# Performance work log

Hardware: AMD Instinct MI355X
Metric: run time of the kernel (lower is better)

Reference implementation:

```python
import jax, jax.numpy as jnp
import numpy as np

N = 100000
E = 3200000
F_IN = 128


def gcn_conv(x, w, b, src, dst, n):
    """PyG GCNConv: out = D^-1/2 (A + I) D^-1/2 (x @ w) + b.
    src/dst already include self loops."""
    xw = x @ w                                   # [N, F_out]
    ones = jnp.ones(src.shape[0], dtype=xw.dtype)
    deg = jax.ops.segment_sum(ones, dst, num_segments=n)   # in-degree incl. self loop
    dinv = jnp.where(deg > 0, jax.lax.rsqrt(deg), 0.0)
    norm = dinv[src] * dinv[dst]                 # [E+N]
    msg = xw[src] * norm[:, None]                # gather + scale
    out = jax.ops.segment_sum(msg, dst, num_segments=n)
    return out + b


def setup_inputs() -> dict:
    key = jax.random.key(0)
    ks = jax.random.split(key, 10)
    x = jax.random.normal(ks[0], (N, F_IN), dtype=jnp.float32)
    edge_index = jax.random.randint(ks[1], (2, E), 0, N, dtype=jnp.int64)
    # Glorot-ish init for weights
    def lin(k, fi, fo):
        return jax.random.normal(k, (fi, fo), dtype=jnp.float32) / np.sqrt(fi)
    return {
        "x": x,
        "edge_index": edge_index,
        "w1": lin(ks[2], F_IN, 64), "b1": jnp.zeros((64,), jnp.float32),
        "w2": lin(ks[3], 64, 32),   "b2": jnp.zeros((32,), jnp.float32),
        "w3": lin(ks[4], 32, 16),   "b3": jnp.zeros((16,), jnp.float32),
        "w_out": lin(ks[5], 16, 1), "b_out": jnp.zeros((1,), jnp.float32),
    }


def reference(x, edge_index, w1, b1, w2, b2, w3, b3, w_out, b_out):
    n = x.shape[0]
    # add self loops once (PyG adds them inside each GCNConv; same graph => same result)
    loop = jnp.arange(n, dtype=edge_index.dtype)
    src = jnp.concatenate([edge_index[0], loop])
    dst = jnp.concatenate([edge_index[1], loop])
    h = jax.nn.relu(gcn_conv(x, w1, b1, src, dst, n))
    h = jax.nn.relu(gcn_conv(h, w2, b2, src, dst, n))
    h = jax.nn.relu(gcn_conv(h, w3, b3, src, dst, n))
    return h @ w_out + b_out  # [N, 1]
```

## Files before the change

### kernel.cpp

```cpp
#include <hip/hip_runtime.h>
#include <hip/hip_bf16.h>


#define NBUCK 391
#define BSHIFT 8
#define CAP 10240
#define TILE 4096

typedef __attribute__((ext_vector_type(2))) unsigned short ushort2v;
typedef __attribute__((ext_vector_type(4))) unsigned short ushort4v;
typedef __attribute__((ext_vector_type(8))) unsigned short ushort8v;
typedef __attribute__((ext_vector_type(8))) _Float16 half8;
typedef __attribute__((ext_vector_type(4))) float f32x4;

__device__ __forceinline__ float bf2f(unsigned short u) {
  union { unsigned int i; float f; } v;
  v.i = ((unsigned int)u) << 16;
  return v.f;
}
__device__ __forceinline__ unsigned short f2bf(float f) {
  union { float f; unsigned int i; } v;
  v.f = f;
  unsigned int r = v.i + 0x7FFF + ((v.i >> 16) & 1);
  return (unsigned short)(r >> 16);
}

static __global__ __launch_bounds__(256) void partition_kernel(
    const int* __restrict__ src, const int* __restrict__ dst,
    int* __restrict__ bucket_cnt, int* __restrict__ part, int E) {
  __shared__ int sorted[TILE];
  __shared__ int hist[512];
  __shared__ int lstart[512];
  __shared__ int cur[512];
  __shared__ int gbase[512];
  __shared__ int sdata[256];
  const int t = threadIdx.x;
  const int base0 = blockIdx.x * TILE;
  hist[t] = 0;
  hist[t + 256] = 0;
  __syncthreads();
  for (int i = t * 4; i < TILE; i += 1024) {
    int gi = base0 + i;
    if (gi + 4 <= E) {
      int4 d = *(const int4*)&dst[gi];
      atomicAdd(&hist[d.x >> BSHIFT], 1);
      atomicAdd(&hist[d.y >> BSHIFT], 1);
      atomicAdd(&hist[d.z >> BSHIFT], 1);
      atomicAdd(&hist[d.w >> BSHIFT], 1);
    } else {
      for (int k = 0; k < 4 && gi + k < E; ++k)
        atomicAdd(&hist[dst[gi + k] >> BSHIFT], 1);
    }
  }
  __syncthreads();
  const int v0 = hist[2 * t], v1 = hist[2 * t + 1];
  const int s = v0 + v1;
  sdata[t] = s;
  __syncthreads();
  int incl = s;
  for (int off = 1; off < 256; off <<= 1) {
    int y = (t >= off) ? sdata[t - off] : 0;
    __syncthreads();
    incl += y;
    sdata[t] = incl;
    __syncthreads();
  }
  const int excl = incl - s;
  lstart[2 * t] = excl;
  lstart[2 * t + 1] = excl + v0;
  cur[2 * t] = 0;
  cur[2 * t + 1] = 0;
  if (2 * t < NBUCK && v0) gbase[2 * t] = atomicAdd(&bucket_cnt[2 * t], v0);
  if (2 * t + 1 < NBUCK && v1)
    gbase[2 * t + 1] = atomicAdd(&bucket_cnt[2 * t + 1], v1);
  __syncthreads();
  for (int i = t * 4; i < TILE; i += 1024) {
    int gi = base0 + i;
    if (gi + 4 <= E) {
      int4 d = *(const int4*)&dst[gi];
      int4 sc = *(const int4*)&src[gi];
      int b0 = d.x >> BSHIFT, b1 = d.y >> BSHIFT;
      int b2 = d.z >> BSHIFT, b3 = d.w >> BSHIFT;
      int p0 = lstart[b0] + atomicAdd(&cur[b0], 1);
      sorted[p0] = ((d.x & 255) << 17) | sc.x;
      int p1 = lstart[b1] + atomicAdd(&cur[b1], 1);
      sorted[p1] = ((d.y & 255) << 17) | sc.y;
      int p2 = lstart[b2] + atomicAdd(&cur[b2], 1);
      sorted[p2] = ((d.z & 255) << 17) | sc.z;
      int p3 = lstart[b3] + atomicAdd(&cur[b3], 1);
      sorted[p3] = ((d.w & 255) << 17) | sc.w;
    } else {
      for (int k = 0; k < 4 && gi + k < E; ++k) {
        int d = dst[gi + k], sc = src[gi + k];
        int b = d >> BSHIFT;
        int pos = lstart[b] + atomicAdd(&cur[b], 1);
        sorted[pos] = ((d & 255) << 17) | sc;
      }
    }
  }
  __syncthreads();
  for (int b = t; b < NBUCK; b += 256) {
    int h = hist[b];
    if (!h) continue;
    int gb = gbase[b];
    int lim = CAP - gb;
    if (lim > h) lim = h;
    const int ls = lstart[b];
    int* dstp = &part[(size_t)b * CAP + gb];
    for (int k = 0; k < lim; ++k) dstp[k] = sorted[ls + k];
  }
}

static __global__ __launch_bounds__(256) void bucket2csr_kernel(
    const int* __restrict__ bucket_cnt, const int* __restrict__ part,
    int* __restrict__ csr_src, int* __restrict__ row_start,
    int* __restrict__ row_end, float* __restrict__ dinv, int n) {
  __shared__ int sorted[CAP];
  __shared__ int hist[256];
  __shared__ int cursor[256];
  __shared__ int sdata[256];
  const int b = blockIdx.x;
  const int t = threadIdx.x;
  const int base = b * CAP;
  int cnt = bucket_cnt[b];
  if (cnt > CAP) cnt = CAP;
  hist[t] = 0;
  __syncthreads();
  int i = t * 4;
  for (; i + 4 <= cnt; i += 1024) {
    int4 v = *(const int4*)&part[base + i];
    atomicAdd(&hist[v.x >> 17], 1);
    atomicAdd(&hist[v.y >> 17], 1);
    atomicAdd(&hist[v.z >> 17], 1);
    atomicAdd(&hist[v.w >> 17], 1);
  }
  for (int k = i; k < cnt && k < i + 4; ++k)
    atomicAdd(&hist[part[base + k] >> 17], 1);
  __syncthreads();
  const int v = hist[t];
  const int pd = (v + 7) & ~7;
  sdata[t] = pd;
  __syncthreads();
  int incl = pd;
  for (int off = 1; off < 256; off <<= 1) {
    int y = (t >= off) ? sdata[t - off] : 0;
    __syncthreads();
    incl += y;
    sdata[t] = incl;
    __syncthreads();
  }
  const int excl = incl - pd;
  const int ptot = sdata[255];
  cursor[t] = excl;
  const int node = b * 256 + t;
  if (node < n) {
    row_start[node] = base + excl;
    row_end[node] = base + excl + pd;
    dinv[node] = rsqrtf((float)(v + 1));
  }
  __syncthreads();
  i = t * 4;
  for (; i + 4 <= cnt; i += 1024) {
    int4 pv = *(const int4*)&part[base + i];
    int p0 = atomicAdd(&cursor[pv.x >> 17], 1);
    sorted[p0] = pv.x & 0x1FFFF;
    int p1 = atomicAdd(&cursor[pv.y >> 17], 1);
    sorted[p1] = pv.y & 0x1FFFF;
    int p2 = atomicAdd(&cursor[pv.z >> 17], 1);
    sorted[p2] = pv.z & 0x1FFFF;
    int p3 = atomicAdd(&cursor[pv.w >> 17], 1);
    sorted[p3] = pv.w & 0x1FFFF;
  }
  for (int k = i; k < cnt && k < i + 4; ++k) {
    int pv = part[base + k];
    int pos = atomicAdd(&cursor[pv >> 17], 1);
    sorted[pos] = pv & 0x1FFFF;
  }
  for (int k = v; k < pd; ++k) sorted[excl + k] = n;
  __syncthreads();
  for (int j = t * 4; j + 4 <= ptot; j += 1024)
    *(int4*)&csr_src[base + j] = *(const int4*)&sorted[j];
}

static __global__ __launch_bounds__(256) void gemm1_mfma_kernel(
    const float* __restrict__ x, const float* __restrict__ w1,
    const float* __restrict__ dinv, unsigned short* __restrict__ xws, int n) {
  __shared__ _Float16 xa[64 * 128];
  __shared__ _Float16 wt[64 * 128];
  const int t = threadIdx.x;
  const int base = blockIdx.x * 64;
  for (int i = t; i < 64 * 16; i += 256) {
    int r = i >> 4, k8 = i & 15;
    int node = base + r;
    float4 a = {0.f, 0.f, 0.f, 0.f}, b = {0.f, 0.f, 0.f, 0.f};
    if (node < n) {
      a = *(const float4*)&x[(size_t)node * 128 + k8 * 8];
      b = *(const float4*)&x[(size_t)node * 128 + k8 * 8 + 4];
    }
    half8 h = {(_Float16)a.x, (_Float16)a.y, (_Float16)a.z, (_Float16)a.w,
               (_Float16)b.x, (_Float16)b.y, (_Float16)b.z, (_Float16)b.w};
    int byte = (r * 256 + k8 * 16) ^ ((r & 7) << 4);
    *(half8*)((char*)xa + byte) = h;
  }
  for (int i = t; i < 128 * 64; i += 256) {
    int k = i >> 6, o = i & 63;
    _Float16 v = (_Float16)w1[i];
    int byte = (o * 256 + k * 2) ^ ((o & 7) << 4);
    *(_Float16*)((char*)wt + byte) = v;
  }
  __syncthreads();
  const int wv = t >> 6;
  const int lane = t & 63;
  const int m = lane & 15;
  const int kg = lane >> 4;
  const int arow = wv * 16 + m;
  f32x4 acc[4] = {{0.f, 0.f, 0.f, 0.f}, {0.f, 0.f, 0.f, 0.f},
                  {0.f, 0.f, 0.f, 0.f}, {0.f, 0.f, 0.f, 0.f}};
#pragma unroll
  for (int ks = 0; ks < 4; ++ks) {
    int k0 = ks * 32 + kg * 8;
    int abyte = (arow * 256 + k0 * 2) ^ ((arow & 7) << 4);
    half8 af = *(const half8*)((const char*)xa + abyte);
#pragma unroll
    for (int nt = 0; nt < 4; ++nt) {
      int o = nt * 16 + m;
      int bbyte = (o * 256 + k0 * 2) ^ ((o & 7) << 4);
      half8 bf = *(const half8*)((const char*)wt + bbyte);
      acc[nt] = __builtin_amdgcn_mfma_f32_16x16x32_f16(af, bf, acc[nt], 0, 0, 0);
    }
  }
#pragma unroll
  for (int r = 0; r < 4; ++r) {
    int node = base + wv * 16 + kg * 4 + r;
    if (node < n) {
      float dv = dinv[node];
#pragma unroll
      for (int nt = 0; nt < 4; ++nt)
        xws[(size_t)node * 64 + nt * 16 + m] = f2bf(dv * acc[nt][r]);
    }
  }
}

template <int F, int FOUT>
static __global__ __launch_bounds__(256) void agg_gemm_kernel(
    const unsigned short* __restrict__ xws, const int* __restrict__ row_start,
    const int* __restrict__ row_end, const int* __restrict__ csr_src,
    const float* __restrict__ dinv, const float* __restrict__ bias,
    const float* __restrict__ W, unsigned short* __restrict__ xws_next, int n) {
  constexpr int GC = F / 8;
  constexpr int LPN = F / 4;
  constexpr int NODES = 256 / LPN;
  constexpr int OUTS = FOUT / LPN;
  __shared__ float ws[F * FOUT];
  __shared__ float hs[NODES][F + 1];
  const int t = threadIdx.x;
  for (int i = t; i < F * FOUT / 4; i += 256)
    *(float4*)&ws[i * 4] = *(const float4*)&W[i * 4];
  const int nl = t / LPN;
  const int l = t % LPN;
  const int c = l % GC;
  const int sub = l / GC;
  const int node = blockIdx.x * NODES + nl;
  const bool valid = node < n;
  const int safe = valid ? node : 0;
  const int start = valid ? row_start[safe] : 0;
  const int end = valid ? row_end[safe] : 0;
  float acc[8] = {0.f, 0.f, 0.f, 0.f, 0.f, 0.f, 0.f, 0.f};
  for (int e = start + sub * 8; e < end; e += 16) {
    int4 sa = *(const int4*)&csr_src[e];
    int4 sb = *(const int4*)&csr_src[e + 4];
    ushort8v v0 = *(const ushort8v*)&xws[(size_t)sa.x * F + c * 8];
    ushort8v v1 = *(const ushort8v*)&xws[(size_t)sa.y * F + c * 8];
    ushort8v v2 = *(const ushort8v*)&xws[(size_t)sa.z * F + c * 8];
    ushort8v v3 = *(const ushort8v*)&xws[(size_t)sa.w * F + c * 8];
    ushort8v v4 = *(const ushort8v*)&xws[(size_t)sb.x * F + c * 8];
    ushort8v v5 = *(const ushort8v*)&xws[(size_t)sb.y * F + c * 8];
    ushort8v v6 = *(const ushort8v*)&xws[(size_t)sb.z * F + c * 8];
    ushort8v v7 = *(const ushort8v*)&xws[(size_t)sb.w * F + c * 8];
#pragma unroll
    for (int j = 0; j < 8; ++j)
      acc[j] += ((bf2f(v0[j]) + bf2f(v1[j])) + (bf2f(v2[j]) + bf2f(v3[j]))) +
                ((bf2f(v4[j]) + bf2f(v5[j])) + (bf2f(v6[j]) + bf2f(v7[j])));
  }
#pragma unroll
  for (int j = 0; j < 8; ++j) acc[j] += __shfl_xor(acc[j], GC);
  const float dv = dinv[safe];
  if (sub == 0) {
    ushort8v sv = *(const ushort8v*)&xws[(size_t)safe * F + c * 8];
#pragma unroll
    for (int j = 0; j < 8; ++j)
      hs[nl][c * 8 + j] =
          fmaxf(dv * (acc[j] + bf2f(sv[j])) + bias[c * 8 + j], 0.f);
  }
  __syncthreads();
  float o[OUTS];
#pragma unroll
  for (int j = 0; j < OUTS; ++j) o[j] = 0.f;
#pragma unroll 4
  for (int k = 0; k < F; ++k) {
    float hv = hs[nl][k];
#pragma unroll
    for (int j = 0; j < OUTS; ++j) o[j] += hv * ws[k * FOUT + l * OUTS + j];
  }
  if (valid) {
    ushort2v r = {f2bf(dv * o[0]), f2bf(dv * o[1])};
    *(ushort2v*)&xws_next[(size_t)node * FOUT + l * OUTS] = r;
  }
}

static __global__ __launch_bounds__(256) void agg_head_kernel(
    const unsigned short* __restrict__ xws, const int* __restrict__ row_start,
    const int* __restrict__ row_end, const int* __restrict__ csr_src,
    const float* __restrict__ dinv, const float* __restrict__ bias,
    float* __restrict__ out, const float* __restrict__ w_out,
    const float* __restrict__ b_out, int n) {
  constexpr int F = 16, NODES = 64;
  const int t = threadIdx.x;
  const int nl = t >> 2;
  const int l = t & 3;
  const int c = l & 1;
  const int sub = l >> 1;
  const int node = blockIdx.x * NODES + nl;
  if (node >= n) return;
  const int start = row_start[node], end = row_end[node];
  float acc[8] = {0.f, 0.f, 0.f, 0.f, 0.f, 0.f, 0.f, 0.f};
  for (int e = start + sub * 8; e < end; e += 16) {
    int4 sa = *(const int4*)&csr_src[e];
    int4 sb = *(const int4*)&csr_src[e + 4];
    ushort8v v0 = *(const ushort8v*)&xws[(size_t)sa.x * F + c * 8];
    ushort8v v1 = *(const ushort8v*)&xws[(size_t)sa.y * F + c * 8];
    ushort8v v2 = *(const ushort8v*)&xws[(size_t)sa.z * F + c * 8];
    ushort8v v3 = *(const ushort8v*)&xws[(size_t)sa.w * F + c * 8];
    ushort8v v4 = *(const ushort8v*)&xws[(size_t)sb.x * F + c * 8];
    ushort8v v5 = *(const ushort8v*)&xws[(size_t)sb.y * F + c * 8];
    ushort8v v6 = *(const ushort8v*)&xws[(size_t)sb.z * F + c * 8];
    ushort8v v7 = *(const ushort8v*)&xws[(size_t)sb.w * F + c * 8];
#pragma unroll
    for (int j = 0; j < 8; ++j)
      acc[j] += ((bf2f(v0[j]) + bf2f(v1[j])) + (bf2f(v2[j]) + bf2f(v3[j]))) +
                ((bf2f(v4[j]) + bf2f(v5[j])) + (bf2f(v6[j]) + bf2f(v7[j])));
  }
#pragma unroll
  for (int j = 0; j < 8; ++j) acc[j] += __shfl_xor(acc[j], 2);
  ushort8v sv = *(const ushort8v*)&xws[(size_t)node * F + c * 8];
  float dv = dinv[node];
  float p = 0.f;
#pragma unroll
  for (int j = 0; j < 8; ++j) {
    float r = fmaxf(dv * (acc[j] + bf2f(sv[j])) + bias[c * 8 + j], 0.f);
    p += r * w_out[c * 8 + j];
  }
  p += __shfl_xor(p, 1);
  if (l == 0) out[node] = p + b_out[0];
}

extern "C" void kernel_launch(void* const* d_in, const int* in_sizes, int n_in,
                              void* d_out, int out_size, void* d_ws, size_t ws_size,
                              hipStream_t stream) {
  const float* x     = (const float*)d_in[0];
  const int*   ei    = (const int*)d_in[1];
  const float* w1    = (const float*)d_in[2];
  const float* b1    = (const float*)d_in[3];
  const float* w2    = (const float*)d_in[4];
  const float* b2    = (const float*)d_in[5];
  const float* w3    = (const float*)d_in[6];
  const float* b3    = (const float*)d_in[7];
  const float* w_out = (const float*)d_in[8];
  const float* b_out = (const float*)d_in[9];
  float* out = (float*)d_out;

  const int n = in_sizes[0] / 128;
  const int E = in_sizes[1] / 2;
  const int* srcA = ei;
  const int* dstA = ei + E;

  char* p = (char*)d_ws;
  auto carve = [&](size_t bytes) {
    void* r = (void*)p;
    p += (bytes + 255) & ~(size_t)255;
    return r;
  };
  const size_t partBytes = (size_t)NBUCK * CAP * 4;
  int*   csr_src    = (int*)carve(partBytes);
  int*   bucket_cnt = (int*)carve((size_t)NBUCK * 4);
  int*   row_start  = (int*)carve((size_t)n * 4);
  int*   row_end    = (int*)carve((size_t)n * 4);
  float* dinv       = (float*)carve((size_t)n * 4);
  char*  regionP    = (char*)carve(partBytes);
  int*   part       = (int*)regionP;
  unsigned short* xws1 = (unsigned short*)regionP;
  unsigned short* xws2 = (unsigned short*)carve((size_t)(n + 1) * 32 * 2);
  unsigned short* xws3 = (unsigned short*)carve((size_t)(n + 1) * 16 * 2);

  hipMemsetAsync(bucket_cnt, 0, (size_t)NBUCK * 4, stream);
  partition_kernel<<<(E + TILE - 1) / TILE, 256, 0, stream>>>(srcA, dstA,
                                                              bucket_cnt, part, E);
  bucket2csr_kernel<<<NBUCK, 256, 0, stream>>>(bucket_cnt, part, csr_src,
                                               row_start, row_end, dinv, n);
  hipMemsetAsync(xws1 + (size_t)n * 64, 0, 64 * 2, stream);
  hipMemsetAsync(xws2 + (size_t)n * 32, 0, 32 * 2, stream);
  hipMemsetAsync(xws3 + (size_t)n * 16, 0, 16 * 2, stream);

  gemm1_mfma_kernel<<<(n + 63) / 64, 256, 0, stream>>>(x, w1, dinv, xws1, n);
  agg_gemm_kernel<64, 32><<<(n + 15) / 16, 256, 0, stream>>>(
      xws1, row_start, row_end, csr_src, dinv, b1, w2, xws2, n);
  agg_gemm_kernel<32, 16><<<(n + 31) / 32, 256, 0, stream>>>(
      xws2, row_start, row_end, csr_src, dinv, b2, w3, xws3, n);
  agg_head_kernel<<<(n + 63) / 64, 256, 0, stream>>>(
      xws3, row_start, row_end, csr_src, dinv, b3, out, w_out, b_out, n);
}
```

Before: 198.1 us.

## Double lanes per node in aggregation, cache edges in registers, fold memsets into kernels

The aggregation kernels now use twice as many lanes per node. Each lane strides 32 edges and the partial sums are combined with an extra shuffle, which adds memory-level parallelism on the gathers. The partition kernel loads src/dst once into registers and reuses them for both histogram and scatter passes instead of re-reading global memory. The three sentinel-row memsets are replaced by writes inside the GEMM/aggregation kernels, saving launch overhead. The risks are fewer nodes per block, more shuffles, and higher register pressure in partition.

```diff
diff --git a/kernel.cpp b/kernel.cpp
--- a/kernel.cpp
+++ b/kernel.cpp
@@ -39,18 +39,27 @@
   hist[t] = 0;
   hist[t + 256] = 0;
   __syncthreads();
-  for (int i = t * 4; i < TILE; i += 1024) {
-    int gi = base0 + i;
+  int4 sv[4], dv[4];
+#pragma unroll
+  for (int j = 0; j < 4; ++j) {
+    int gi = base0 + t * 4 + j * 1024;
     if (gi + 4 <= E) {
-      int4 d = *(const int4*)&dst[gi];
-      atomicAdd(&hist[d.x >> BSHIFT], 1);
-      atomicAdd(&hist[d.y >> BSHIFT], 1);
-      atomicAdd(&hist[d.z >> BSHIFT], 1);
-      atomicAdd(&hist[d.w >> BSHIFT], 1);
+      sv[j] = *(const int4*)&src[gi];
+      dv[j] = *(const int4*)&dst[gi];
     } else {
-      for (int k = 0; k < 4 && gi + k < E; ++k)
-        atomicAdd(&hist[dst[gi + k] >> BSHIFT], 1);
-    }
+      sv[j].x = (gi + 0 < E) ? src[gi + 0] : -1;
+      sv[j].y = (gi + 1 < E) ? src[gi + 1] : -1;
+      sv[j].z = (gi + 2 < E) ? src[gi + 2] : -1;
+      sv[j].w = (gi + 3 < E) ? src[gi + 3] : -1;
+      dv[j].x = (gi + 0 < E) ? dst[gi + 0] : 0;
+      dv[j].y = (gi + 1 < E) ? dst[gi + 1] : 0;
+      dv[j].z = (gi + 2 < E) ? dst[gi + 2] : 0;
+      dv[j].w = (gi + 3 < E) ? dst[gi + 3] : 0;
+    }
+    if (sv[j].x >= 0) atomicAdd(&hist[dv[j].x >> BSHIFT], 1);
+    if (sv[j].y >= 0) atomicAdd(&hist[dv[j].y >> BSHIFT], 1);
+    if (sv[j].z >= 0) atomicAdd(&hist[dv[j].z >> BSHIFT], 1);
+    if (sv[j].w >= 0) atomicAdd(&hist[dv[j].w >> BSHIFT], 1);
   }
   __syncthreads();
   const int v0 = hist[2 * t], v1 = hist[2 * t + 1];
@@ -74,28 +83,23 @@
   if (2 * t + 1 < NBUCK && v1)
     gbase[2 * t + 1] = atomicAdd(&bucket_cnt[2 * t + 1], v1);
   __syncthreads();
-  for (int i = t * 4; i < TILE; i += 1024) {
-    int gi = base0 + i;
-    if (gi + 4 <= E) {
-      int4 d = *(const int4*)&dst[gi];
-      int4 sc = *(const int4*)&src[gi];
-      int b0 = d.x >> BSHIFT, b1 = d.y >> BSHIFT;
-      int b2 = d.z >> BSHIFT, b3 = d.w >> BSHIFT;
-      int p0 = lstart[b0] + atomicAdd(&cur[b0], 1);
-      sorted[p0] = ((d.x & 255) << 17) | sc.x;
-      int p1 = lstart[b1] + atomicAdd(&cur[b1], 1);
-      sorted[p1] = ((d.y & 255) << 17) | sc.y;
-      int p2 = lstart[b2] + atomicAdd(&cur[b2], 1);
-      sorted[p2] = ((d.z & 255) << 17) | sc.z;
-      int p3 = lstart[b3] + atomicAdd(&cur[b3], 1);
-      sorted[p3] = ((d.w & 255) << 17) | sc.w;
-    } else {
-      for (int k = 0; k < 4 && gi + k < E; ++k) {
-        int d = dst[gi + k], sc = src[gi + k];
-        int b = d >> BSHIFT;
-        int pos = lstart[b] + atomicAdd(&cur[b], 1);
-        sorted[pos] = ((d & 255) << 17) | sc;
-      }
+#pragma unroll
+  for (int j = 0; j < 4; ++j) {
+    if (sv[j].x >= 0) {
+      int b = dv[j].x >> BSHIFT;
+      sorted[lstart[b] + atomicAdd(&cur[b], 1)] = ((dv[j].x & 255) << 17) | sv[j].x;
+    }
+    if (sv[j].y >= 0) {
+      int b = dv[j].y >> BSHIFT;
+      sorted[lstart[b] + atomicAdd(&cur[b], 1)] = ((dv[j].y & 255) << 17) | sv[j].y;
+    }
+    if (sv[j].z >= 0) {
+      int b = dv[j].z >> BSHIFT;
+      sorted[lstart[b] + atomicAdd(&cur[b], 1)] = ((dv[j].z & 255) << 17) | sv[j].z;
+    }
+    if (sv[j].w >= 0) {
+      int b = dv[j].w >> BSHIFT;
+      sorted[lstart[b] + atomicAdd(&cur[b], 1)] = ((dv[j].w & 255) << 17) | sv[j].w;
     }
   }
   __syncthreads();
@@ -189,6 +193,10 @@
   __shared__ _Float16 wt[64 * 128];
   const int t = threadIdx.x;
   const int base = blockIdx.x * 64;
+  if (blockIdx.x == 0 && t < 8) {
+    ushort8v z = {0, 0, 0, 0, 0, 0, 0, 0};
+    *(ushort8v*)&xws[(size_t)n * 64 + t * 8] = z;
+  }
   for (int i = t; i < 64 * 16; i += 256) {
     int r = i >> 4, k8 = i & 15;
     int node = base + r;
@@ -248,12 +256,16 @@
     const float* __restrict__ dinv, const float* __restrict__ bias,
     const float* __restrict__ W, unsigned short* __restrict__ xws_next, int n) {
   constexpr int GC = F / 8;
-  constexpr int LPN = F / 4;
+  constexpr int LPN = F / 2;
   constexpr int NODES = 256 / LPN;
-  constexpr int OUTS = FOUT / LPN;
+  static_assert(FOUT == LPN, "epilogue writes 1 out per lane");
   __shared__ float ws[F * FOUT];
   __shared__ float hs[NODES][F + 1];
   const int t = threadIdx.x;
+  if (blockIdx.x == 0 && t < FOUT / 8) {
+    ushort8v z = {0, 0, 0, 0, 0, 0, 0, 0};
+    *(ushort8v*)&xws_next[(size_t)n * FOUT + t * 8] = z;
+  }
   for (int i = t; i < F * FOUT / 4; i += 256)
     *(float4*)&ws[i * 4] = *(const float4*)&W[i * 4];
   const int nl = t / LPN;
@@ -266,7 +278,7 @@
   const int start = valid ? row_start[safe] : 0;
   const int end = valid ? row_end[safe] : 0;
   float acc[8] = {0.f, 0.f, 0.f, 0.f, 0.f, 0.f, 0.f, 0.f};
-  for (int e = start + sub * 8; e < end; e += 16) {
+  for (int e = start + sub * 8; e < end; e += 32) {
     int4 sa = *(const int4*)&csr_src[e];
     int4 sb = *(const int4*)&csr_src[e + 4];
     ushort8v v0 = *(const ushort8v*)&xws[(size_t)sa.x * F + c * 8];
@@ -283,7 +295,10 @@
                 ((bf2f(v4[j]) + bf2f(v5[j])) + (bf2f(v6[j]) + bf2f(v7[j])));
   }
 #pragma unroll
-  for (int j = 0; j < 8; ++j) acc[j] += __shfl_xor(acc[j], GC);
+  for (int j = 0; j < 8; ++j) {
+    acc[j] += __shfl_xor(acc[j], GC);
+    acc[j] += __shfl_xor(acc[j], 2 * GC);
+  }
   const float dv = dinv[safe];
   if (sub == 0) {
     ushort8v sv = *(const ushort8v*)&xws[(size_t)safe * F + c * 8];
@@ -293,19 +308,10 @@
           fmaxf(dv * (acc[j] + bf2f(sv[j])) + bias[c * 8 + j], 0.f);
   }
   __syncthreads();
-  float o[OUTS];
-#pragma unroll
-  for (int j = 0; j < OUTS; ++j) o[j] = 0.f;
+  float o = 0.f;
 #pragma unroll 4
-  for (int k = 0; k < F; ++k) {
-    float hv = hs[nl][k];
-#pragma unroll
-    for (int j = 0; j < OUTS; ++j) o[j] += hv * ws[k * FOUT + l * OUTS + j];
-  }
-  if (valid) {
-    ushort2v r = {f2bf(dv * o[0]), f2bf(dv * o[1])};
-    *(ushort2v*)&xws_next[(size_t)node * FOUT + l * OUTS] = r;
-  }
+  for (int k = 0; k < F; ++k) o += hs[nl][k] * ws[k * FOUT + l];
+  if (valid) xws_next[(size_t)node * FOUT + l] = f2bf(dv * o);
 }
 
 static __global__ __launch_bounds__(256) void agg_head_kernel(
@@ -314,17 +320,17 @@
     const float* __restrict__ dinv, const float* __restrict__ bias,
     float* __restrict__ out, const float* __restrict__ w_out,
     const float* __restrict__ b_out, int n) {
-  constexpr int F = 16, NODES = 64;
+  constexpr int F = 16, NODES = 32;
   const int t = threadIdx.x;
-  const int nl = t >> 2;
-  const int l = t & 3;
+  const int nl = t >> 3;
+  const int l = t & 7;
   const int c = l & 1;
   const int sub = l >> 1;
   const int node = blockIdx.x * NODES + nl;
   if (node >= n) return;
   const int start = row_start[node], end = row_end[node];
   float acc[8] = {0.f, 0.f, 0.f, 0.f, 0.f, 0.f, 0.f, 0.f};
-  for (int e = start + sub * 8; e < end; e += 16) {
+  for (int e = start + sub * 8; e < end; e += 32) {
     int4 sa = *(const int4*)&csr_src[e];
     int4 sb = *(const int4*)&csr_src[e + 4];
     ushort8v v0 = *(const ushort8v*)&xws[(size_t)sa.x * F + c * 8];
@@ -341,7 +347,10 @@
                 ((bf2f(v4[j]) + bf2f(v5[j])) + (bf2f(v6[j]) + bf2f(v7[j])));
   }
 #pragma unroll
-  for (int j = 0; j < 8; ++j) acc[j] += __shfl_xor(acc[j], 2);
+  for (int j = 0; j < 8; ++j) {
+    acc[j] += __shfl_xor(acc[j], 2);
+    acc[j] += __shfl_xor(acc[j], 4);
+  }
   ushort8v sv = *(const ushort8v*)&xws[(size_t)node * F + c * 8];
   float dv = dinv[node];
   float p = 0.f;
@@ -397,15 +406,12 @@
                                                               bucket_cnt, part, E);
   bucket2csr_kernel<<<NBUCK, 256, 0, stream>>>(bucket_cnt, part, csr_src,
                                                row_start, row_end, dinv, n);
-  hipMemsetAsync(xws1 + (size_t)n * 64, 0, 64 * 2, stream);
-  hipMemsetAsync(xws2 + (size_t)n * 32, 0, 32 * 2, stream);
-  hipMemsetAsync(xws3 + (size_t)n * 16, 0, 16 * 2, stream);
 
   gemm1_mfma_kernel<<<(n + 63) / 64, 256, 0, stream>>>(x, w1, dinv, xws1, n);
-  agg_gemm_kernel<64, 32><<<(n + 15) / 16, 256, 0, stream>>>(
+  agg_gemm_kernel<64, 32><<<(n + 7) / 8, 256, 0, stream>>>(
       xws1, row_start, row_end, csr_src, dinv, b1, w2, xws2, n);
-  agg_gemm_kernel<32, 16><<<(n + 31) / 32, 256, 0, stream>>>(
+  agg_gemm_kernel<32, 16><<<(n + 15) / 16, 256, 0, stream>>>(
       xws2, row_start, row_end, csr_src, dinv, b2, w3, xws3, n);
-  agg_head_kernel<<<(n + 63) / 64, 256, 0, stream>>>(
+  agg_head_kernel<<<(n + 31) / 32, 256, 0, stream>>>(
       xws3, row_start, row_end, csr_src, dinv, b3, out, w_out, b_out, n);
 }
```

Measured after the change: 190.2 us. 1.04x faster.
